# Performance work log

Measured on AMD Instinct MI355X. Metric: run time of the kernel, lower is better.

The kernel has to match this reference:

```python
import jax, jax.numpy as jnp
import numpy as np

N_NODES = 100000
N_EDGES = 100000
D = 256
N_SIDE = 2  # rel_list = [side_a, side_b, rel_c, rel_d]
N_REL = 2


def setup_inputs() -> dict:
    key = jax.random.key(0)
    ks = jax.random.split(key, 7)
    h = jax.random.normal(ks[0], (N_NODES, D), dtype=jnp.float32)
    src_idx = jax.random.randint(ks[1], (N_SIDE + N_REL, N_EDGES), 0, N_NODES)
    dst_idx = jax.random.randint(ks[2], (N_SIDE + N_REL, N_EDGES), 0, N_NODES)
    # shared bilinear matrix R (nn.Linear(D, D, bias=False): y = x @ R_W.T)
    R_W = jax.random.normal(ks[3], (D, D), dtype=jnp.float32) * (1.0 / np.sqrt(D))
    # per-'side*' diagonal parameters (xavier over [D,1] then squeeze)
    d_side = jax.random.normal(ks[4], (N_SIDE, D), dtype=jnp.float32)
    # per-regular-relation Linear weights (with bias)
    W_rel = jax.random.normal(ks[5], (N_REL, D, D), dtype=jnp.float32) * (1.0 / np.sqrt(D))
    b_rel = jax.random.normal(ks[6], (N_REL, D), dtype=jnp.float32) * 0.01
    return {"h": h, "src_idx": src_idx, "dst_idx": dst_idx,
            "R_W": R_W, "d_side": d_side, "W_rel": W_rel, "b_rel": b_rel}


def reference(h, src_idx, dst_idx, R_W, d_side, W_rel, b_rel):
    # --- 'side*' edge types: score = (((h_u * d) @ R_W.T) * d) . h_v ---
    hu_s = h[src_idx[:N_SIDE]]            # [S, E, D] gather
    hv_s = h[dst_idx[:N_SIDE]]            # [S, E, D]
    lft = hu_s * d_side[:, None, :]       # [S, E, D]
    lft = jnp.einsum('sed,fd->sef', lft, R_W)  # Linear, no bias
    lft = lft * d_side[:, None, :]
    score_side = jnp.einsum('sed,sed->se', lft, hv_s)  # [S, E]

    # --- regular edge types: score = (h_u @ W.T + b) . h_v ---
    hu_r = h[src_idx[N_SIDE:]]            # [R, E, D]
    hv_r = h[dst_idx[N_SIDE:]]            # [R, E, D]
    lft_r = jnp.einsum('red,rfd->ref', hu_r, W_rel) + b_rel[:, None, :]
    score_rel = jnp.einsum('red,red->re', lft_r, hv_r)  # [R, E]

    return jnp.concatenate([score_side, score_rel], axis=0)  # [S+R, E]
```

## Files before the change

### kernel.cpp

```cpp
#include <hip/hip_runtime.h>
#include <stdint.h>

#define NNODES 100000
#define NEDGES 100000
#define DIM    256
#define NCH    4
#define ET     32
#define RS     260

typedef short bf16x8 __attribute__((ext_vector_type(8)));
typedef float f32x4  __attribute__((ext_vector_type(4)));
typedef uint32_t u32x4 __attribute__((ext_vector_type(4)));

__device__ __forceinline__ short f2bf_rn(float x) {
    union { float f; uint32_t u; } v; v.f = x;
    uint32_t u = v.u;
    uint32_t r = u + 0x7fffu + ((u >> 16) & 1u);
    return (short)(r >> 16);
}
__device__ __forceinline__ float bf2f(short s) {
    union { float f; uint32_t u; } v;
    v.u = ((uint32_t)(unsigned short)s) << 16;
    return v.f;
}
__device__ __forceinline__ float asf(uint32_t u) {
    union { float f; uint32_t u; } v; v.u = u; return v.f;
}

__global__ void prep_B(const float* __restrict__ RW,
                       const float* __restrict__ dside,
                       const float* __restrict__ Wrel,
                       short* __restrict__ Bh, short* __restrict__ Bl) {
    int t = blockIdx.x * blockDim.x + threadIdx.x;
    if (t >= NCH * 8 * 16 * 64) return;
    int lane = t & 63;
    int ft   = (t >> 6) & 15;
    int kc   = (t >> 10) & 7;
    int c    = t >> 13;
    int quad = lane >> 4, col = lane & 15;
    int f     = ft * 16 + col;
    int kbase = kc * 32 + quad * 8;

    bf16x8 vh, vl;
#pragma unroll
    for (int j = 0; j < 8; ++j) {
        int k = kbase + j;
        float val;
        if (c < 2) {
            val = dside[c * DIM + f] * RW[f * DIM + k] * dside[c * DIM + k];
        } else {
            val = Wrel[(size_t)(c - 2) * DIM * DIM + f * DIM + k];
        }
        short hi = f2bf_rn(val);
        float rem = val - bf2f(hi);
        vh[j] = hi;
        vl[j] = f2bf_rn(rem);
    }
    ((bf16x8*)Bh)[t] = vh;
    ((bf16x8*)Bl)[t] = vl;
}

__global__ __launch_bounds__(256, 2)
void edge_kernel(const float* __restrict__ hmat,
                 const int* __restrict__ src_idx,
                 const int* __restrict__ dst_idx,
                 const float* __restrict__ brel,
                 const short* __restrict__ Bh_sw,
                 const short* __restrict__ Bl_sw,
                 float* __restrict__ out) {
    const int c    = blockIdx.y;
    const int e0   = blockIdx.x * ET;
    const int tid  = threadIdx.x;
    const int w    = tid >> 6;
    const int lane = tid & 63;
    const int quad = lane >> 4, col = lane & 15;

    __shared__ uint32_t s_row[ET * RS];
    __shared__ uint32_t s_src[ET];
    __shared__ uint32_t s_dst[ET];
    __shared__ float    red[4][ET];

    if (tid < ET) {
        int idx = e0 + tid;
        int si = 0, di = 0;
        if (idx < NEDGES) {
            si = src_idx[(size_t)c * NEDGES + idx];
            di = dst_idx[(size_t)c * NEDGES + idx];
        }
        s_src[tid] = (uint32_t)si;
        s_dst[tid] = (uint32_t)di;
    }
    __syncthreads();

#pragma unroll
    for (int i = 0; i < 8; ++i) {
        int lr = w * 8 + i;
        const float* rb = hmat + (size_t)s_src[lr] * DIM;
        f32x4 x = *(const f32x4*)(rb + lane * 4);
        u32x4 o;
#pragma unroll
        for (int j = 0; j < 4; ++j) {
            short hi = f2bf_rn(x[j]);
            short lo = f2bf_rn(x[j] - bf2f(hi));
            o[j] = ((uint32_t)(unsigned short)hi << 16) | (uint32_t)(unsigned short)lo;
        }
        *(u32x4*)&s_row[lr * RS + lane * 4] = o;
    }
    __syncthreads();

    f32x4 acc[2][4];
#pragma unroll
    for (int i = 0; i < 2; ++i)
#pragma unroll
        for (int j = 0; j < 4; ++j) acc[i][j] = (f32x4){0.f, 0.f, 0.f, 0.f};

    const bf16x8* Bh = (const bf16x8*)Bh_sw;
    const bf16x8* Bl = (const bf16x8*)Bl_sw;

#pragma unroll
    for (int kc = 0; kc < 8; ++kc) {
        bf16x8 Ah[2], Al[2];
#pragma unroll
        for (int mt = 0; mt < 2; ++mt) {
            const uint32_t* p = &s_row[(mt * 16 + col) * RS + kc * 32 + quad * 8];
            u32x4 q0 = *(const u32x4*)p;
            u32x4 q1 = *(const u32x4*)(p + 4);
            bf16x8 ah, al;
#pragma unroll
            for (int j = 0; j < 4; ++j) {
                ah[j]     = (short)(q0[j] >> 16);
                al[j]     = (short)(q0[j] & 0xffffu);
                ah[4 + j] = (short)(q1[j] >> 16);
                al[4 + j] = (short)(q1[j] & 0xffffu);
            }
            Ah[mt] = ah;
            Al[mt] = al;
        }
        int fb = ((c * 8 + kc) * 16 + w * 4) * 64 + lane;
#pragma unroll
        for (int ft = 0; ft < 4; ++ft) {
            bf16x8 bh = Bh[fb + ft * 64];
            bf16x8 bl = Bl[fb + ft * 64];
#pragma unroll
            for (int mt = 0; mt < 2; ++mt) {
                acc[mt][ft] = __builtin_amdgcn_mfma_f32_16x16x32_bf16(Ah[mt], bh, acc[mt][ft], 0, 0, 0);
                acc[mt][ft] = __builtin_amdgcn_mfma_f32_16x16x32_bf16(Ah[mt], bl, acc[mt][ft], 0, 0, 0);
                acc[mt][ft] = __builtin_amdgcn_mfma_f32_16x16x32_bf16(Al[mt], bh, acc[mt][ft], 0, 0, 0);
            }
        }
    }
    __syncthreads();

#pragma unroll
    for (int i = 0; i < 8; ++i) {
        int lr = w * 8 + i;
        const float* rb = hmat + (size_t)s_dst[lr] * DIM;
        f32x4 x = *(const f32x4*)(rb + lane * 4);
        u32x4 o;
#pragma unroll
        for (int j = 0; j < 4; ++j) {
            union { float f; uint32_t u; } cv; cv.f = x[j]; o[j] = cv.u;
        }
        *(u32x4*)&s_row[lr * RS + lane * 4] = o;
    }
    __syncthreads();

    float bias[4];
#pragma unroll
    for (int ft = 0; ft < 4; ++ft) {
        int f = w * 64 + ft * 16 + col;
        bias[ft] = (c >= 2) ? brel[(size_t)(c - 2) * DIM + f] : 0.f;
    }

    float psum[2][4];
#pragma unroll
    for (int mt = 0; mt < 2; ++mt) {
#pragma unroll
        for (int r = 0; r < 4; ++r) {
            int el = mt * 16 + quad * 4 + r;
            float s = 0.f;
#pragma unroll
            for (int ft = 0; ft < 4; ++ft) {
                int f = w * 64 + ft * 16 + col;
                float v = asf(s_row[el * RS + f]);
                s += (acc[mt][ft][r] + bias[ft]) * v;
            }
            psum[mt][r] = s;
        }
    }

#pragma unroll
    for (int off = 1; off < 16; off <<= 1) {
#pragma unroll
        for (int mt = 0; mt < 2; ++mt)
#pragma unroll
            for (int r = 0; r < 4; ++r)
                psum[mt][r] += __shfl_xor(psum[mt][r], off, 64);
    }
    if (col == 0) {
#pragma unroll
        for (int mt = 0; mt < 2; ++mt)
#pragma unroll
            for (int r = 0; r < 4; ++r)
                red[w][mt * 16 + quad * 4 + r] = psum[mt][r];
    }
    __syncthreads();

    if (tid < ET) {
        int idx = e0 + tid;
        if (idx < NEDGES) {
            float s = red[0][tid] + red[1][tid] + red[2][tid] + red[3][tid];
            out[(size_t)c * NEDGES + idx] = s;
        }
    }
}

extern "C" void kernel_launch(void* const* d_in, const int* in_sizes, int n_in,
                              void* d_out, int out_size, void* d_ws, size_t ws_size,
                              hipStream_t stream) {
    const float* hmat  = (const float*)d_in[0];
    const int*   src   = (const int*)d_in[1];
    const int*   dst   = (const int*)d_in[2];
    const float* RW    = (const float*)d_in[3];
    const float* dside = (const float*)d_in[4];
    const float* Wrel  = (const float*)d_in[5];
    const float* brel  = (const float*)d_in[6];
    float* out = (float*)d_out;

    const size_t nB = (size_t)NCH * DIM * DIM;
    short* Bh = (short*)d_ws;
    short* Bl = Bh + nB;

    prep_B<<<dim3((NCH * 8 * 16 * 64) / 256), dim3(256), 0, stream>>>(RW, dside, Wrel, Bh, Bl);

    dim3 grid((NEDGES + ET - 1) / ET, NCH);
    edge_kernel<<<grid, dim3(256), 0, stream>>>(hmat, src, dst, brel, Bh, Bl, out);
}
```

Before: 334.5 us.

## Pre-convert node features to fp16 and drop split-A MFMA term

```diff
diff --git a/kernel.cpp b/kernel.cpp
--- a/kernel.cpp
+++ b/kernel.cpp
@@ -6,67 +6,66 @@
 #define DIM    256
 #define NCH    4
 #define ET     32
-#define RS     260
-
-typedef short bf16x8 __attribute__((ext_vector_type(8)));
+#define RSF    264
+
+typedef _Float16 f16x8 __attribute__((ext_vector_type(8)));
+typedef _Float16 f16x4 __attribute__((ext_vector_type(4)));
 typedef float f32x4  __attribute__((ext_vector_type(4)));
-typedef uint32_t u32x4 __attribute__((ext_vector_type(4)));
-
-__device__ __forceinline__ short f2bf_rn(float x) {
-    union { float f; uint32_t u; } v; v.f = x;
-    uint32_t u = v.u;
-    uint32_t r = u + 0x7fffu + ((u >> 16) & 1u);
-    return (short)(r >> 16);
+
+__global__ void prep_fused(const float* __restrict__ RW,
+                           const float* __restrict__ dside,
+                           const float* __restrict__ Wrel,
+                           const float* __restrict__ h,
+                           _Float16* __restrict__ Bh, _Float16* __restrict__ Bl,
+                           _Float16* __restrict__ H16) {
+    if (blockIdx.x < 128) {
+        int t = blockIdx.x * blockDim.x + threadIdx.x;
+        int lane = t & 63;
+        int ft   = (t >> 6) & 15;
+        int kc   = (t >> 10) & 7;
+        int c    = t >> 13;
+        int quad = lane >> 4, col = lane & 15;
+        int f     = ft * 16 + col;
+        int kbase = kc * 32 + quad * 8;
+
+        f16x8 vh, vl;
+#pragma unroll
+        for (int j = 0; j < 8; ++j) {
+            int k = kbase + j;
+            float val;
+            if (c < 2) {
+                val = dside[c * DIM + f] * RW[f * DIM + k] * dside[c * DIM + k];
+            } else {
+                val = Wrel[(size_t)(c - 2) * DIM * DIM + f * DIM + k];
+            }
+            _Float16 hi = (_Float16)val;
+            vh[j] = hi;
+            vl[j] = (_Float16)(val - (float)hi);
+        }
+        ((f16x8*)Bh)[t] = vh;
+        ((f16x8*)Bl)[t] = vl;
+    } else {
+        int u = (blockIdx.x - 128) * blockDim.x + threadIdx.x;
+        if (u >= NNODES * DIM / 8) return;
+        f32x4 x0 = ((const f32x4*)h)[2 * u];
+        f32x4 x1 = ((const f32x4*)h)[2 * u + 1];
+        f16x8 o;
+#pragma unroll
+        for (int j = 0; j < 4; ++j) {
+            o[j]     = (_Float16)x0[j];
+            o[4 + j] = (_Float16)x1[j];
+        }
+        ((f16x8*)H16)[u] = o;
+    }
 }
-__device__ __forceinline__ float bf2f(short s) {
-    union { float f; uint32_t u; } v;
-    v.u = ((uint32_t)(unsigned short)s) << 16;
-    return v.f;
-}
-__device__ __forceinline__ float asf(uint32_t u) {
-    union { float f; uint32_t u; } v; v.u = u; return v.f;
-}
-
-__global__ void prep_B(const float* __restrict__ RW,
-                       const float* __restrict__ dside,
-                       const float* __restrict__ Wrel,
-                       short* __restrict__ Bh, short* __restrict__ Bl) {
-    int t = blockIdx.x * blockDim.x + threadIdx.x;
-    if (t >= NCH * 8 * 16 * 64) return;
-    int lane = t & 63;
-    int ft   = (t >> 6) & 15;
-    int kc   = (t >> 10) & 7;
-    int c    = t >> 13;
-    int quad = lane >> 4, col = lane & 15;
-    int f     = ft * 16 + col;
-    int kbase = kc * 32 + quad * 8;
-
-    bf16x8 vh, vl;
-#pragma unroll
-    for (int j = 0; j < 8; ++j) {
-        int k = kbase + j;
-        float val;
-        if (c < 2) {
-            val = dside[c * DIM + f] * RW[f * DIM + k] * dside[c * DIM + k];
-        } else {
-            val = Wrel[(size_t)(c - 2) * DIM * DIM + f * DIM + k];
-        }
-        short hi = f2bf_rn(val);
-        float rem = val - bf2f(hi);
-        vh[j] = hi;
-        vl[j] = f2bf_rn(rem);
-    }
-    ((bf16x8*)Bh)[t] = vh;
-    ((bf16x8*)Bl)[t] = vl;
-}
 
 __global__ __launch_bounds__(256, 2)
-void edge_kernel(const float* __restrict__ hmat,
+void edge_kernel(const _Float16* __restrict__ H16,
                  const int* __restrict__ src_idx,
                  const int* __restrict__ dst_idx,
                  const float* __restrict__ brel,
-                 const short* __restrict__ Bh_sw,
-                 const short* __restrict__ Bl_sw,
+                 const _Float16* __restrict__ Bh_sw,
+                 const _Float16* __restrict__ Bl_sw,
                  float* __restrict__ out) {
     const int c    = blockIdx.y;
     const int e0   = blockIdx.x * ET;
@@ -75,7 +74,7 @@
     const int lane = tid & 63;
     const int quad = lane >> 4, col = lane & 15;
 
-    __shared__ uint32_t s_row[ET * RS];
+    __shared__ __align__(16) _Float16 s_row[ET * RSF];
     __shared__ uint32_t s_src[ET];
     __shared__ uint32_t s_dst[ET];
     __shared__ float    red[4][ET];
@@ -95,16 +94,9 @@
 #pragma unroll
     for (int i = 0; i < 8; ++i) {
         int lr = w * 8 + i;
-        const float* rb = hmat + (size_t)s_src[lr] * DIM;
-        f32x4 x = *(const f32x4*)(rb + lane * 4);
-        u32x4 o;
-#pragma unroll
-        for (int j = 0; j < 4; ++j) {
-            short hi = f2bf_rn(x[j]);
-            short lo = f2bf_rn(x[j] - bf2f(hi));
-            o[j] = ((uint32_t)(unsigned short)hi << 16) | (uint32_t)(unsigned short)lo;
-        }
-        *(u32x4*)&s_row[lr * RS + lane * 4] = o;
+        const _Float16* rb = H16 + (size_t)s_src[lr] * DIM;
+        f16x4 x = *(const f16x4*)(rb + lane * 4);
+        *(f16x4*)&s_row[lr * RSF + lane * 4] = x;
     }
     __syncthreads();
 
@@ -114,38 +106,25 @@
 #pragma unroll
         for (int j = 0; j < 4; ++j) acc[i][j] = (f32x4){0.f, 0.f, 0.f, 0.f};
 
-    const bf16x8* Bh = (const bf16x8*)Bh_sw;
-    const bf16x8* Bl = (const bf16x8*)Bl_sw;
+    const f16x8* Bh = (const f16x8*)Bh_sw;
+    const f16x8* Bl = (const f16x8*)Bl_sw;
 
 #pragma unroll
     for (int kc = 0; kc < 8; ++kc) {
-        bf16x8 Ah[2], Al[2];
-#pragma unroll
-        for (int mt = 0; mt < 2; ++mt) {
-            const uint32_t* p = &s_row[(mt * 16 + col) * RS + kc * 32 + quad * 8];
-            u32x4 q0 = *(const u32x4*)p;
-            u32x4 q1 = *(const u32x4*)(p + 4);
-            bf16x8 ah, al;
-#pragma unroll
-            for (int j = 0; j < 4; ++j) {
-                ah[j]     = (short)(q0[j] >> 16);
-                al[j]     = (short)(q0[j] & 0xffffu);
-                ah[4 + j] = (short)(q1[j] >> 16);
-                al[4 + j] = (short)(q1[j] & 0xffffu);
-            }
-            Ah[mt] = ah;
-            Al[mt] = al;
-        }
+        f16x8 A[2];
+#pragma unroll
+        for (int mt = 0; mt < 2; ++mt)
+            A[mt] = *(const f16x8*)&s_row[(mt * 16 + col) * RSF + kc * 32 + quad * 8];
+
         int fb = ((c * 8 + kc) * 16 + w * 4) * 64 + lane;
 #pragma unroll
         for (int ft = 0; ft < 4; ++ft) {
-            bf16x8 bh = Bh[fb + ft * 64];
-            bf16x8 bl = Bl[fb + ft * 64];
+            f16x8 bh = Bh[fb + ft * 64];
+            f16x8 bl = Bl[fb + ft * 64];
 #pragma unroll
             for (int mt = 0; mt < 2; ++mt) {
-                acc[mt][ft] = __builtin_amdgcn_mfma_f32_16x16x32_bf16(Ah[mt], bh, acc[mt][ft], 0, 0, 0);
-                acc[mt][ft] = __builtin_amdgcn_mfma_f32_16x16x32_bf16(Ah[mt], bl, acc[mt][ft], 0, 0, 0);
-                acc[mt][ft] = __builtin_amdgcn_mfma_f32_16x16x32_bf16(Al[mt], bh, acc[mt][ft], 0, 0, 0);
+                acc[mt][ft] = __builtin_amdgcn_mfma_f32_16x16x32_f16(A[mt], bh, acc[mt][ft], 0, 0, 0);
+                acc[mt][ft] = __builtin_amdgcn_mfma_f32_16x16x32_f16(A[mt], bl, acc[mt][ft], 0, 0, 0);
             }
         }
     }
@@ -154,14 +133,9 @@
 #pragma unroll
     for (int i = 0; i < 8; ++i) {
         int lr = w * 8 + i;
-        const float* rb = hmat + (size_t)s_dst[lr] * DIM;
-        f32x4 x = *(const f32x4*)(rb + lane * 4);
-        u32x4 o;
-#pragma unroll
-        for (int j = 0; j < 4; ++j) {
-            union { float f; uint32_t u; } cv; cv.f = x[j]; o[j] = cv.u;
-        }
-        *(u32x4*)&s_row[lr * RS + lane * 4] = o;
+        const _Float16* rb = H16 + (size_t)s_dst[lr] * DIM;
+        f16x4 x = *(const f16x4*)(rb + lane * 4);
+        *(f16x4*)&s_row[lr * RSF + lane * 4] = x;
     }
     __syncthreads();
 
@@ -182,7 +156,7 @@
 #pragma unroll
             for (int ft = 0; ft < 4; ++ft) {
                 int f = w * 64 + ft * 16 + col;
-                float v = asf(s_row[el * RS + f]);
+                float v = (float)s_row[el * RSF + f];
                 s += (acc[mt][ft][r] + bias[ft]) * v;
             }
             psum[mt][r] = s;
@@ -228,11 +202,14 @@
     float* out = (float*)d_out;
 
     const size_t nB = (size_t)NCH * DIM * DIM;
-    short* Bh = (short*)d_ws;
-    short* Bl = Bh + nB;
-
-    prep_B<<<dim3((NCH * 8 * 16 * 64) / 256), dim3(256), 0, stream>>>(RW, dside, Wrel, Bh, Bl);
+    _Float16* Bh  = (_Float16*)d_ws;
+    _Float16* Bl  = Bh + nB;
+    _Float16* H16 = Bl + nB;
+
+    const int convBlocks = (NNODES * DIM / 8 + 255) / 256;
+    prep_fused<<<dim3(128 + convBlocks), dim3(256), 0, stream>>>(
+        RW, dside, Wrel, hmat, Bh, Bl, H16);
 
     dim3 grid((NEDGES + ET - 1) / ET, NCH);
-    edge_kernel<<<grid, dim3(256), 0, stream>>>(hmat, src, dst, brel, Bh, Bl, out);
+    edge_kernel<<<grid, dim3(256), 0, stream>>>(H16, src, dst, brel, Bh, Bl, out);
 }
```

New measurement: 311.8 us. -6.8%, faster.
